# Performance work log

Hardware: AMD Instinct MI355X
Metric: run time of the kernel (lower is better)

Reference implementation:

```python
import jax, jax.numpy as jnp
import numpy as np

B, N, F = 8, 8192, 64
NPOINT, NSAMPLE = 2048, 32
RADIUS = 0.2
MLP = [64, 64, 128]
EPS = 1e-5
SLOPE = 0.2


def fps(pts_t, npoint):
    """Furthest point sampling. pts_t: (B,N,3) -> (B,npoint) int32 indices."""
    b, n, _ = pts_t.shape
    def body(carry, _):
        dist, far = carry
        centroid = jnp.take_along_axis(pts_t, far[:, None, None], axis=1)  # (B,1,3)
        d = jnp.sum((pts_t - centroid) ** 2, axis=-1)                      # (B,N)
        dist = jnp.minimum(dist, d)
        return (dist, jnp.argmax(dist, axis=-1).astype(jnp.int32)), far
    init = (jnp.full((b, n), 1e10, pts_t.dtype), jnp.zeros((b,), jnp.int32))
    _, idxs = jax.lax.scan(body, init, None, length=npoint)
    return jnp.transpose(idxs)  # (B,npoint)


def ball_query(pts_t, q_t, radius, k):
    """pts_t: (B,N,3), q_t: (B,S,3) -> (B,S,k) int32; first in-ball index fills empty slots."""
    n = pts_t.shape[1]
    d = (jnp.sum(q_t ** 2, -1, keepdims=True) + jnp.sum(pts_t ** 2, -1)[:, None, :]
         - 2.0 * jnp.einsum('bsc,bnc->bsn', q_t, pts_t))
    idx = jnp.where(d < radius * radius, jnp.arange(n, dtype=jnp.int32)[None, None, :], n)
    idx = -jax.lax.top_k(-idx, k)[0]  # k smallest indices, ascending order
    first = idx[:, :, :1]
    return jnp.where(idx == n, first, idx)


def _layer(x, w, b, g, bb, m, v):
    # 1x1 conv + BatchNorm(eval) + LeakyReLU(0.2); x: (B,S,K,Cin) -> (B,S,K,Cout)
    y = jnp.einsum('bskc,oc->bsko', x, w) + b
    y = (y - m) * (g * jax.lax.rsqrt(v + EPS)) + bb
    return jnp.where(y > 0, y, SLOPE * y)


def _forward(features, points, params):
    pts_t = jnp.transpose(points, (0, 2, 1))  # (B,N,3)
    fidx = fps(jax.lax.stop_gradient(pts_t), NPOINT)                    # (B,S)
    new_xyz_t = jnp.take_along_axis(pts_t, fidx[:, :, None], axis=1)    # (B,S,3)
    idx = ball_query(jax.lax.stop_gradient(pts_t), jax.lax.stop_gradient(new_xyz_t), RADIUS, NSAMPLE)
    gather = jax.vmap(lambda p, i: p[i])
    grouped_xyz = gather(pts_t, idx) - new_xyz_t[:, :, None, :]         # (B,S,K,3)
    grouped_feat = gather(jnp.transpose(features, (0, 2, 1)), idx)      # (B,S,K,F)
    x = jnp.concatenate([grouped_xyz, grouped_feat], axis=-1)           # (B,S,K,3+F)
    for (w, b, g, bb, m, v) in params:
        x = _layer(x, w, b, g, bb, m, v)
    new_features = jnp.transpose(jnp.max(x, axis=2), (0, 2, 1))         # (B,mlp[-1],S)
    new_xyz = jnp.transpose(new_xyz_t, (0, 2, 1))                       # (B,3,S)
    return new_features, new_xyz


def setup_inputs() -> dict:
    key = jax.random.key(0)
    ks = jax.random.split(key, 32)
    inp = {
        'features': jax.random.normal(ks[0], (B, F, N), jnp.float32),
        'points': jax.random.uniform(ks[1], (B, 3, N), jnp.float32),
    }
    chans = [F + 3] + MLP
    j = 2
    for i in range(len(MLP)):
        cin, cout = chans[i], chans[i + 1]
        inp[f'w{i+1}'] = jax.random.normal(ks[j], (cout, cin), jnp.float32) / np.sqrt(cin).astype(np.float32); j += 1
        inp[f'b{i+1}'] = jax.random.normal(ks[j], (cout,), jnp.float32) * 0.1; j += 1
        inp[f'g{i+1}'] = jax.random.uniform(ks[j], (cout,), jnp.float32, 0.5, 1.5); j += 1
        inp[f'bb{i+1}'] = jax.random.normal(ks[j], (cout,), jnp.float32) * 0.1; j += 1
        inp[f'm{i+1}'] = jax.random.normal(ks[j], (cout,), jnp.float32) * 0.1; j += 1
        inp[f'v{i+1}'] = jax.random.uniform(ks[j], (cout,), jnp.float32, 0.5, 1.5); j += 1
    return inp


def reference(features, points, w1, b1, g1, bb1, m1, v1, w2, b2, g2, bb2, m2, v2, w3, b3, g3, bb3, m3, v3):
    params = [(w1, b1, g1, bb1, m1, v1), (w2, b2, g2, bb2, m2, v2), (w3, b3, g3, bb3, m3, v3)]
    return _forward(features, points, params)
```

## Files before the change

### kernel.cpp

```cpp
#include <hip/hip_runtime.h>
#include <cstdint>
#include <cstddef>

#define NBATCH  8
#define NPTS    8192
#define NFEAT   64
#define NPOINT  2048
#define NSAMPLE 32

__global__ void prep_kernel(const float* __restrict__ w1, const float* __restrict__ b1,
                            const float* __restrict__ g1, const float* __restrict__ bb1,
                            const float* __restrict__ m1, const float* __restrict__ v1,
                            const float* __restrict__ w2, const float* __restrict__ b2,
                            const float* __restrict__ g2, const float* __restrict__ bb2,
                            const float* __restrict__ m2, const float* __restrict__ v2,
                            const float* __restrict__ w3, const float* __restrict__ b3,
                            const float* __restrict__ g3, const float* __restrict__ bb3,
                            const float* __restrict__ m3, const float* __restrict__ v3,
                            float* __restrict__ wbuf) {
    int i = blockIdx.x * 256 + threadIdx.x;
    if (i < 4288) {
        int o = i & 63, c = i >> 6;
        float s = g1[o] / sqrtf(v1[o] + 1e-5f);
        wbuf[i] = w1[o * 67 + c] * s;
    } else if (i < 4352) {
        int o = i - 4288;
        float s = g1[o] / sqrtf(v1[o] + 1e-5f);
        wbuf[i] = (b1[o] - m1[o]) * s + bb1[o];
    } else if (i < 8448) {
        int j = i - 4352; int o = j & 63, c = j >> 6;
        float s = g2[o] / sqrtf(v2[o] + 1e-5f);
        wbuf[i] = w2[o * 64 + c] * s;
    } else if (i < 8512) {
        int o = i - 8448;
        float s = g2[o] / sqrtf(v2[o] + 1e-5f);
        wbuf[i] = (b2[o] - m2[o]) * s + bb2[o];
    } else if (i < 16704) {
        int j = i - 8512; int o = j & 127, c = j >> 7;
        float s = g3[o] / sqrtf(v3[o] + 1e-5f);
        wbuf[i] = w3[o * 64 + c] * s;
    } else if (i < 16832) {
        int o = i - 16704;
        float s = g3[o] / sqrtf(v3[o] + 1e-5f);
        wbuf[i] = (b3[o] - m3[o]) * s + bb3[o];
    }
}

__global__ __launch_bounds__(512, 2) void fps_kernel(const float* __restrict__ points,
                                                     int* __restrict__ fidx) {
    const int b = blockIdx.x;
    const int tid = threadIdx.x;
    const int lane = tid & 63;
    const float* __restrict__ pxg = points + (size_t)b * 3 * NPTS;
    const float* __restrict__ pyg = pxg + NPTS;
    const float* __restrict__ pzg = pyg + NPTS;

    __shared__ float lx[NPTS];
    __shared__ float ly[NPTS];
    __shared__ float lz[NPTS];
    __shared__ float pv[2][8];
    __shared__ int   pi[2][8];

    float px[16], py[16], pz[16], dd[16];
#pragma unroll
    for (int j = 0; j < 16; ++j) {
        int n = tid + 512 * j;
        px[j] = pxg[n]; py[j] = pyg[n]; pz[j] = pzg[n];
        lx[n] = px[j];  ly[n] = py[j];  lz[n] = pz[j];
        dd[j] = 1e10f;
    }
    if (tid == 0) fidx[b * NPOINT + 0] = 0;
    __syncthreads();
    int w = 0;
    for (int i = 1; i < NPOINT; ++i) {
        const float cx = lx[w], cy = ly[w], cz = lz[w];
        float bestd = -1.0f; int besti = 0;
#pragma unroll
        for (int j = 0; j < 16; ++j) {
            float dx = __fsub_rn(px[j], cx);
            float dy = __fsub_rn(py[j], cy);
            float dz = __fsub_rn(pz[j], cz);
            float d  = __fadd_rn(__fadd_rn(__fmul_rn(dx, dx), __fmul_rn(dy, dy)),
                                 __fmul_rn(dz, dz));
            float nd = fminf(dd[j], d);
            dd[j] = nd;
            bool better = (nd > bestd);
            bestd = better ? nd : bestd;
            besti = better ? (tid + 512 * j) : besti;
        }
#pragma unroll
        for (int off = 32; off >= 1; off >>= 1) {
            float od = __shfl_down(bestd, off);
            int   oi = __shfl_down(besti, off);
            bool take = (od > bestd) || (od == bestd && oi < besti);
            bestd = take ? od : bestd;
            besti = take ? oi : besti;
        }
        const int par = i & 1;
        if (lane == 0) { pv[par][tid >> 6] = bestd; pi[par][tid >> 6] = besti; }
        __syncthreads();
        float fd = (lane < 8) ? pv[par][lane] : -1.0f;
        int   fi = (lane < 8) ? pi[par][lane] : 0x7fffffff;
#pragma unroll
        for (int off = 4; off >= 1; off >>= 1) {
            float od = __shfl_down(fd, off);
            int   oi = __shfl_down(fi, off);
            bool take = (od > fd) || (od == fd && oi < fi);
            fd = take ? od : fd;
            fi = take ? oi : fi;
        }
        w = __shfl(fi, 0);
        if (tid == 0) fidx[b * NPOINT + i] = w;
    }
}

__global__ __launch_bounds__(256) void bq_kernel(const float* __restrict__ points,
                                                 const int* __restrict__ fidx,
                                                 int* __restrict__ ballidx,
                                                 float* __restrict__ out_xyz) {
    const int lane = threadIdx.x & 63;
    const int gw = (blockIdx.x << 2) + (threadIdx.x >> 6);
    const int b = gw >> 11;
    const int q = gw & 2047;
    const float* __restrict__ pxg = points + (size_t)b * 3 * NPTS;
    const float* __restrict__ pyg = pxg + NPTS;
    const float* __restrict__ pzg = pyg + NPTS;
    const int qi = fidx[b * NPOINT + q];
    const float qx = pxg[qi], qy = pyg[qi], qz = pzg[qi];
    const float qq = __fadd_rn(__fadd_rn(__fmul_rn(qx, qx), __fmul_rn(qy, qy)),
                               __fmul_rn(qz, qz));
    int* __restrict__ out = ballidx + ((size_t)(b * NPOINT + q)) * NSAMPLE;
    int have = 0;
    int first = -1;
    for (int base = 0; base < NPTS && have < NSAMPLE; base += 64) {
        const int n = base + lane;
        float x = pxg[n], y = pyg[n], z = pzg[n];
        float pp = __fadd_rn(__fadd_rn(__fmul_rn(x, x), __fmul_rn(y, y)), __fmul_rn(z, z));
        float qp = __builtin_fmaf(qz, z, __builtin_fmaf(qy, y, __fmul_rn(qx, x)));
        float d  = __fsub_rn(__fadd_rn(qq, pp), __fmul_rn(2.0f, qp));
        bool inb = d < 0.04f;
        unsigned long long mask = __ballot(inb);
        if (mask) {
            if (first < 0) first = base + __ffsll(mask) - 1;
            if (inb) {
                int slot = have + (int)__popcll(mask & ((1ull << lane) - 1ull));
                if (slot < NSAMPLE) out[slot] = n;
            }
            have += (int)__popcll(mask);
        }
    }
    for (int s = have + lane; s < NSAMPLE; s += 64) out[s] = first;
    if (lane == 0) {
        float* o0 = out_xyz + (size_t)b * 3 * NPOINT + q;
        o0[0] = qx; o0[NPOINT] = qy; o0[2 * NPOINT] = qz;
    }
}

#define XS 36
__global__ __launch_bounds__(256) void mlp_kernel(const float* __restrict__ feats,
                                                  const float* __restrict__ points,
                                                  const int* __restrict__ fidx,
                                                  const int* __restrict__ ballidx,
                                                  const float* __restrict__ wbuf,
                                                  float* __restrict__ out) {
    __shared__ float xT[67 * XS];
    __shared__ float yA[64 * XS];
    __shared__ float wl[8192];
    __shared__ float bl[128];
    __shared__ int   il[32];
    __shared__ float qv[3];
    const int tid = threadIdx.x;
    const int bq = blockIdx.x;
    const int b = bq >> 11, q = bq & 2047;
    const float* __restrict__ pb = points + (size_t)b * 3 * NPTS;

    if (tid < 32) il[tid] = ballidx[((size_t)(b * NPOINT + q)) * NSAMPLE + tid];
    if (tid < 3)  qv[tid] = pb[(size_t)tid * NPTS + fidx[b * NPOINT + q]];
    for (int i = tid; i < 4288; i += 256) wl[i] = wbuf[i];
    if (tid < 64) bl[tid] = wbuf[4288 + tid];
    __syncthreads();

    if (tid < 32) {
        int n = il[tid];
        xT[0 * XS + tid] = pb[n] - qv[0];
        xT[1 * XS + tid] = pb[NPTS + n] - qv[1];
        xT[2 * XS + tid] = pb[2 * NPTS + n] - qv[2];
    }
    {
        int k = tid & 31, fg = tid >> 5;
        int n = il[k];
        const float* fb = feats + ((size_t)b * NFEAT + fg * 8) * NPTS + n;
#pragma unroll
        for (int u = 0; u < 8; ++u) xT[(3 + fg * 8 + u) * XS + k] = fb[(size_t)u * NPTS];
    }
    __syncthreads();

    const int o = tid & 63, kb = tid >> 6;
    float acc[8];
#pragma unroll
    for (int j = 0; j < 8; ++j) acc[j] = 0.f;
    for (int c = 0; c < 67; ++c) {
        float wv = wl[c * 64 + o];
        const float4* xp = (const float4*)&xT[c * XS + kb * 8];
        float4 a0 = xp[0], a1 = xp[1];
        acc[0] = fmaf(wv, a0.x, acc[0]); acc[1] = fmaf(wv, a0.y, acc[1]);
        acc[2] = fmaf(wv, a0.z, acc[2]); acc[3] = fmaf(wv, a0.w, acc[3]);
        acc[4] = fmaf(wv, a1.x, acc[4]); acc[5] = fmaf(wv, a1.y, acc[5]);
        acc[6] = fmaf(wv, a1.z, acc[6]); acc[7] = fmaf(wv, a1.w, acc[7]);
    }
    {
        float t = bl[o];
#pragma unroll
        for (int j = 0; j < 8; ++j) {
            float y = acc[j] + t;
            y = y > 0.f ? y : 0.2f * y;
            yA[o * XS + kb * 8 + j] = y;
        }
    }
    __syncthreads();
    for (int i = tid; i < 4096; i += 256) wl[i] = wbuf[4352 + i];
    if (tid < 64) bl[tid] = wbuf[8448 + tid];
    __syncthreads();

#pragma unroll
    for (int j = 0; j < 8; ++j) acc[j] = 0.f;
    for (int c = 0; c < 64; ++c) {
        float wv = wl[c * 64 + o];
        const float4* xp = (const float4*)&yA[c * XS + kb * 8];
        float4 a0 = xp[0], a1 = xp[1];
        acc[0] = fmaf(wv, a0.x, acc[0]); acc[1] = fmaf(wv, a0.y, acc[1]);
        acc[2] = fmaf(wv, a0.z, acc[2]); acc[3] = fmaf(wv, a0.w, acc[3]);
        acc[4] = fmaf(wv, a1.x, acc[4]); acc[5] = fmaf(wv, a1.y, acc[5]);
        acc[6] = fmaf(wv, a1.z, acc[6]); acc[7] = fmaf(wv, a1.w, acc[7]);
    }
    {
        float t = bl[o];
#pragma unroll
        for (int j = 0; j < 8; ++j) {
            float y = acc[j] + t;
            y = y > 0.f ? y : 0.2f * y;
            xT[o * XS + kb * 8 + j] = y;
        }
    }
    __syncthreads();
    for (int i = tid; i < 8192; i += 256) wl[i] = wbuf[8512 + i];
    if (tid < 128) bl[tid] = wbuf[16704 + tid];
    __syncthreads();

    const int o3 = tid & 127, kb3 = tid >> 7;
    float a3[16];
#pragma unroll
    for (int j = 0; j < 16; ++j) a3[j] = 0.f;
    for (int c = 0; c < 64; ++c) {
        float wv = wl[c * 128 + o3];
        const float4* xp = (const float4*)&xT[c * XS + kb3 * 16];
        float4 x0 = xp[0], x1 = xp[1], x2 = xp[2], x3 = xp[3];
        a3[0]  = fmaf(wv, x0.x, a3[0]);  a3[1]  = fmaf(wv, x0.y, a3[1]);
        a3[2]  = fmaf(wv, x0.z, a3[2]);  a3[3]  = fmaf(wv, x0.w, a3[3]);
        a3[4]  = fmaf(wv, x1.x, a3[4]);  a3[5]  = fmaf(wv, x1.y, a3[5]);
        a3[6]  = fmaf(wv, x1.z, a3[6]);  a3[7]  = fmaf(wv, x1.w, a3[7]);
        a3[8]  = fmaf(wv, x2.x, a3[8]);  a3[9]  = fmaf(wv, x2.y, a3[9]);
        a3[10] = fmaf(wv, x2.z, a3[10]); a3[11] = fmaf(wv, x2.w, a3[11]);
        a3[12] = fmaf(wv, x3.x, a3[12]); a3[13] = fmaf(wv, x3.y, a3[13]);
        a3[14] = fmaf(wv, x3.z, a3[14]); a3[15] = fmaf(wv, x3.w, a3[15]);
    }
    {
        float t = bl[o3];
        float m = -3.4e38f;
#pragma unroll
        for (int j = 0; j < 16; ++j) {
            float y = a3[j] + t;
            y = y > 0.f ? y : 0.2f * y;
            m = fmaxf(m, y);
        }
        yA[o3 * 2 + kb3] = m;
    }
    __syncthreads();
    if (tid < 128) {
        float r = fmaxf(yA[tid * 2], yA[tid * 2 + 1]);
        out[((size_t)b * 128 + tid) * NPOINT + q] = r;
    }
}

extern "C" void kernel_launch(void* const* d_in, const int* in_sizes, int n_in,
                              void* d_out, int out_size, void* d_ws, size_t ws_size,
                              hipStream_t stream) {
    (void)in_sizes; (void)n_in; (void)out_size; (void)ws_size;
    const float* feats  = (const float*)d_in[0];
    const float* points = (const float*)d_in[1];
    const float* w1  = (const float*)d_in[2];
    const float* b1  = (const float*)d_in[3];
    const float* g1  = (const float*)d_in[4];
    const float* bb1 = (const float*)d_in[5];
    const float* m1  = (const float*)d_in[6];
    const float* v1  = (const float*)d_in[7];
    const float* w2  = (const float*)d_in[8];
    const float* b2  = (const float*)d_in[9];
    const float* g2  = (const float*)d_in[10];
    const float* bb2 = (const float*)d_in[11];
    const float* m2  = (const float*)d_in[12];
    const float* v2  = (const float*)d_in[13];
    const float* w3  = (const float*)d_in[14];
    const float* b3  = (const float*)d_in[15];
    const float* g3  = (const float*)d_in[16];
    const float* bb3 = (const float*)d_in[17];
    const float* m3  = (const float*)d_in[18];
    const float* v3  = (const float*)d_in[19];

    float* out = (float*)d_out;
    char*  ws  = (char*)d_ws;
    int*   fidx    = (int*)ws;
    int*   ballidx = (int*)(ws + 65536);
    float* wbuf    = (float*)(ws + 65536 + 2097152);
    float* out_xyz = out + (size_t)NBATCH * 128 * NPOINT;

    hipLaunchKernelGGL(prep_kernel, dim3(66), dim3(256), 0, stream,
                       w1, b1, g1, bb1, m1, v1, w2, b2, g2, bb2, m2, v2,
                       w3, b3, g3, bb3, m3, v3, wbuf);
    hipLaunchKernelGGL(fps_kernel, dim3(NBATCH), dim3(512), 0, stream, points, fidx);
    hipLaunchKernelGGL(bq_kernel, dim3(16384 / 4), dim3(256), 0, stream,
                       points, fidx, ballidx, out_xyz);
    hipLaunchKernelGGL(mlp_kernel, dim3(NBATCH * NPOINT), dim3(256), 0, stream,
                       feats, points, fidx, ballidx, wbuf, out);
}
```

Before: 3.262 ms.

## Process two query centroids per MLP block to amortize weight loads

```diff
diff --git a/kernel.cpp b/kernel.cpp
--- a/kernel.cpp
+++ b/kernel.cpp
@@ -156,129 +156,137 @@
     }
 }
 
-#define XS 36
+#define XS2 68
 __global__ __launch_bounds__(256) void mlp_kernel(const float* __restrict__ feats,
                                                   const float* __restrict__ points,
                                                   const int* __restrict__ fidx,
                                                   const int* __restrict__ ballidx,
                                                   const float* __restrict__ wbuf,
                                                   float* __restrict__ out) {
-    __shared__ float xT[67 * XS];
-    __shared__ float yA[64 * XS];
-    __shared__ float wl[8192];
+    __shared__ __align__(16) float xT[67 * XS2];
+    __shared__ __align__(16) float yA[64 * XS2];
+    __shared__ __align__(16) float wl[8192];
     __shared__ float bl[128];
-    __shared__ int   il[32];
-    __shared__ float qv[3];
+    __shared__ int   il[64];
+    __shared__ float qv[6];
     const int tid = threadIdx.x;
-    const int bq = blockIdx.x;
-    const int b = bq >> 11, q = bq & 2047;
+    const int blk = blockIdx.x;
+    const int b = blk >> 10;
+    const int q0 = (blk & 1023) * 2;
     const float* __restrict__ pb = points + (size_t)b * 3 * NPTS;
-
-    if (tid < 32) il[tid] = ballidx[((size_t)(b * NPOINT + q)) * NSAMPLE + tid];
-    if (tid < 3)  qv[tid] = pb[(size_t)tid * NPTS + fidx[b * NPOINT + q]];
-    for (int i = tid; i < 4288; i += 256) wl[i] = wbuf[i];
+    const float4* __restrict__ wb4 = (const float4*)wbuf;
+
+    if (tid < 64)
+        il[tid] = ballidx[((size_t)(b * NPOINT + q0 + (tid >> 5))) * NSAMPLE + (tid & 31)];
+    if (tid < 6) {
+        int qq_ = tid / 3, dim = tid % 3;
+        qv[tid] = pb[(size_t)dim * NPTS + fidx[b * NPOINT + q0 + qq_]];
+    }
+    for (int i = tid; i < 1072; i += 256) ((float4*)wl)[i] = wb4[i];
     if (tid < 64) bl[tid] = wbuf[4288 + tid];
     __syncthreads();
 
-    if (tid < 32) {
-        int n = il[tid];
-        xT[0 * XS + tid] = pb[n] - qv[0];
-        xT[1 * XS + tid] = pb[NPTS + n] - qv[1];
-        xT[2 * XS + tid] = pb[2 * NPTS + n] - qv[2];
+    if (tid < 64) {
+        int n = il[tid], qsel = tid >> 5;
+        xT[0 * XS2 + tid] = pb[n] - qv[qsel * 3 + 0];
+        xT[1 * XS2 + tid] = pb[NPTS + n] - qv[qsel * 3 + 1];
+        xT[2 * XS2 + tid] = pb[2 * NPTS + n] - qv[qsel * 3 + 2];
     }
     {
-        int k = tid & 31, fg = tid >> 5;
+        int k = tid & 63, fg = tid >> 6;
         int n = il[k];
-        const float* fb = feats + ((size_t)b * NFEAT + fg * 8) * NPTS + n;
-#pragma unroll
-        for (int u = 0; u < 8; ++u) xT[(3 + fg * 8 + u) * XS + k] = fb[(size_t)u * NPTS];
-    }
-    __syncthreads();
-
-    const int o = tid & 63, kb = tid >> 6;
-    float acc[8];
-#pragma unroll
-    for (int j = 0; j < 8; ++j) acc[j] = 0.f;
+        const float* fb = feats + ((size_t)b * NFEAT + fg * 16) * NPTS + n;
+#pragma unroll
+        for (int u = 0; u < 16; ++u) xT[(3 + fg * 16 + u) * XS2 + k] = fb[(size_t)u * NPTS];
+    }
+    __syncthreads();
+
+    const int o = tid & 63, w = tid >> 6;
+    float acc[16];
+#pragma unroll
+    for (int j = 0; j < 16; ++j) acc[j] = 0.f;
     for (int c = 0; c < 67; ++c) {
         float wv = wl[c * 64 + o];
-        const float4* xp = (const float4*)&xT[c * XS + kb * 8];
-        float4 a0 = xp[0], a1 = xp[1];
-        acc[0] = fmaf(wv, a0.x, acc[0]); acc[1] = fmaf(wv, a0.y, acc[1]);
-        acc[2] = fmaf(wv, a0.z, acc[2]); acc[3] = fmaf(wv, a0.w, acc[3]);
-        acc[4] = fmaf(wv, a1.x, acc[4]); acc[5] = fmaf(wv, a1.y, acc[5]);
-        acc[6] = fmaf(wv, a1.z, acc[6]); acc[7] = fmaf(wv, a1.w, acc[7]);
+        const float4* xp = (const float4*)&xT[c * XS2 + w * 16];
+        float4 a0 = xp[0], a1 = xp[1], a2 = xp[2], a3v = xp[3];
+        acc[0]  = fmaf(wv, a0.x, acc[0]);  acc[1]  = fmaf(wv, a0.y, acc[1]);
+        acc[2]  = fmaf(wv, a0.z, acc[2]);  acc[3]  = fmaf(wv, a0.w, acc[3]);
+        acc[4]  = fmaf(wv, a1.x, acc[4]);  acc[5]  = fmaf(wv, a1.y, acc[5]);
+        acc[6]  = fmaf(wv, a1.z, acc[6]);  acc[7]  = fmaf(wv, a1.w, acc[7]);
+        acc[8]  = fmaf(wv, a2.x, acc[8]);  acc[9]  = fmaf(wv, a2.y, acc[9]);
+        acc[10] = fmaf(wv, a2.z, acc[10]); acc[11] = fmaf(wv, a2.w, acc[11]);
+        acc[12] = fmaf(wv, a3v.x, acc[12]); acc[13] = fmaf(wv, a3v.y, acc[13]);
+        acc[14] = fmaf(wv, a3v.z, acc[14]); acc[15] = fmaf(wv, a3v.w, acc[15]);
     }
     {
         float t = bl[o];
 #pragma unroll
-        for (int j = 0; j < 8; ++j) {
+        for (int j = 0; j < 16; ++j) {
             float y = acc[j] + t;
             y = y > 0.f ? y : 0.2f * y;
-            yA[o * XS + kb * 8 + j] = y;
-        }
-    }
-    __syncthreads();
-    for (int i = tid; i < 4096; i += 256) wl[i] = wbuf[4352 + i];
+            yA[o * XS2 + w * 16 + j] = y;
+        }
+    }
+    __syncthreads();
+    for (int i = tid; i < 1024; i += 256) ((float4*)wl)[i] = wb4[1088 + i];
     if (tid < 64) bl[tid] = wbuf[8448 + tid];
     __syncthreads();
 
 #pragma unroll
-    for (int j = 0; j < 8; ++j) acc[j] = 0.f;
+    for (int j = 0; j < 16; ++j) acc[j] = 0.f;
     for (int c = 0; c < 64; ++c) {
         float wv = wl[c * 64 + o];
-        const float4* xp = (const float4*)&yA[c * XS + kb * 8];
-        float4 a0 = xp[0], a1 = xp[1];
-        acc[0] = fmaf(wv, a0.x, acc[0]); acc[1] = fmaf(wv, a0.y, acc[1]);
-        acc[2] = fmaf(wv, a0.z, acc[2]); acc[3] = fmaf(wv, a0.w, acc[3]);
-        acc[4] = fmaf(wv, a1.x, acc[4]); acc[5] = fmaf(wv, a1.y, acc[5]);
-        acc[6] = fmaf(wv, a1.z, acc[6]); acc[7] = fmaf(wv, a1.w, acc[7]);
+        const float4* xp = (const float4*)&yA[c * XS2 + w * 16];
+        float4 a0 = xp[0], a1 = xp[1], a2 = xp[2], a3v = xp[3];
+        acc[0]  = fmaf(wv, a0.x, acc[0]);  acc[1]  = fmaf(wv, a0.y, acc[1]);
+        acc[2]  = fmaf(wv, a0.z, acc[2]);  acc[3]  = fmaf(wv, a0.w, acc[3]);
+        acc[4]  = fmaf(wv, a1.x, acc[4]);  acc[5]  = fmaf(wv, a1.y, acc[5]);
+        acc[6]  = fmaf(wv, a1.z, acc[6]);  acc[7]  = fmaf(wv, a1.w, acc[7]);
+        acc[8]  = fmaf(wv, a2.x, acc[8]);  acc[9]  = fmaf(wv, a2.y, acc[9]);
+        acc[10] = fmaf(wv, a2.z, acc[10]); acc[11] = fmaf(wv, a2.w, acc[11]);
+        acc[12] = fmaf(wv, a3v.x, acc[12]); acc[13] = fmaf(wv, a3v.y, acc[13]);
+        acc[14] = fmaf(wv, a3v.z, acc[14]); acc[15] = fmaf(wv, a3v.w, acc[15]);
     }
     {
         float t = bl[o];
 #pragma unroll
-        for (int j = 0; j < 8; ++j) {
+        for (int j = 0; j < 16; ++j) {
             float y = acc[j] + t;
             y = y > 0.f ? y : 0.2f * y;
-            xT[o * XS + kb * 8 + j] = y;
-        }
-    }
-    __syncthreads();
-    for (int i = tid; i < 8192; i += 256) wl[i] = wbuf[8512 + i];
+            xT[o * XS2 + w * 16 + j] = y;
+        }
+    }
+    __syncthreads();
+    for (int i = tid; i < 2048; i += 256) ((float4*)wl)[i] = wb4[2128 + i];
     if (tid < 128) bl[tid] = wbuf[16704 + tid];
     __syncthreads();
 
     const int o3 = tid & 127, kb3 = tid >> 7;
-    float a3[16];
-#pragma unroll
-    for (int j = 0; j < 16; ++j) a3[j] = 0.f;
+    float a3[32];
+#pragma unroll
+    for (int j = 0; j < 32; ++j) a3[j] = 0.f;
     for (int c = 0; c < 64; ++c) {
         float wv = wl[c * 128 + o3];
-        const float4* xp = (const float4*)&xT[c * XS + kb3 * 16];
-        float4 x0 = xp[0], x1 = xp[1], x2 = xp[2], x3 = xp[3];
-        a3[0]  = fmaf(wv, x0.x, a3[0]);  a3[1]  = fmaf(wv, x0.y, a3[1]);
-        a3[2]  = fmaf(wv, x0.z, a3[2]);  a3[3]  = fmaf(wv, x0.w, a3[3]);
-        a3[4]  = fmaf(wv, x1.x, a3[4]);  a3[5]  = fmaf(wv, x1.y, a3[5]);
-        a3[6]  = fmaf(wv, x1.z, a3[6]);  a3[7]  = fmaf(wv, x1.w, a3[7]);
-        a3[8]  = fmaf(wv, x2.x, a3[8]);  a3[9]  = fmaf(wv, x2.y, a3[9]);
-        a3[10] = fmaf(wv, x2.z, a3[10]); a3[11] = fmaf(wv, x2.w, a3[11]);
-        a3[12] = fmaf(wv, x3.x, a3[12]); a3[13] = fmaf(wv, x3.y, a3[13]);
-        a3[14] = fmaf(wv, x3.z, a3[14]); a3[15] = fmaf(wv, x3.w, a3[15]);
+        const float4* xp = (const float4*)&xT[c * XS2 + kb3 * 32];
+#pragma unroll
+        for (int g = 0; g < 8; ++g) {
+            float4 x = xp[g];
+            a3[g * 4 + 0] = fmaf(wv, x.x, a3[g * 4 + 0]);
+            a3[g * 4 + 1] = fmaf(wv, x.y, a3[g * 4 + 1]);
+            a3[g * 4 + 2] = fmaf(wv, x.z, a3[g * 4 + 2]);
+            a3[g * 4 + 3] = fmaf(wv, x.w, a3[g * 4 + 3]);
+        }
     }
     {
         float t = bl[o3];
         float m = -3.4e38f;
 #pragma unroll
-        for (int j = 0; j < 16; ++j) {
+        for (int j = 0; j < 32; ++j) {
             float y = a3[j] + t;
             y = y > 0.f ? y : 0.2f * y;
             m = fmaxf(m, y);
         }
-        yA[o3 * 2 + kb3] = m;
-    }
-    __syncthreads();
-    if (tid < 128) {
-        float r = fmaxf(yA[tid * 2], yA[tid * 2 + 1]);
-        out[((size_t)b * 128 + tid) * NPOINT + q] = r;
+        out[((size_t)b * 128 + o3) * NPOINT + q0 + kb3] = m;
     }
 }
 
@@ -320,6 +328,6 @@
     hipLaunchKernelGGL(fps_kernel, dim3(NBATCH), dim3(512), 0, stream, points, fidx);
     hipLaunchKernelGGL(bq_kernel, dim3(16384 / 4), dim3(256), 0, stream,
                        points, fidx, ballidx, out_xyz);
-    hipLaunchKernelGGL(mlp_kernel, dim3(NBATCH * NPOINT), dim3(256), 0, stream,
+    hipLaunchKernelGGL(mlp_kernel, dim3(NBATCH * 1024), dim3(256), 0, stream,
                        feats, points, fidx, ballidx, wbuf, out);
 }
```

New measurement: 3.224 ms. No clear change (-1.2%).
